# Kernel tuning notes

Measured on AMD Instinct MI355X. Metric: run time of the kernel, lower is better.

Reference implementation:

```python
import jax, jax.numpy as jnp
import numpy as np

B, S, D, H = 2, 2048, 2048, 16
HD = D // H  # 128
L = 10  # adapter_len


def setup_inputs() -> dict:
    key = jax.random.key(0)
    ks = jax.random.split(key, 8)
    x = jax.random.normal(ks[0], (B, S, D), dtype=jnp.float32)
    wq = jax.random.normal(ks[1], (D, D), dtype=jnp.float32) * 0.02
    wk = jax.random.normal(ks[2], (D, D), dtype=jnp.float32) * 0.02
    wv = jax.random.normal(ks[3], (D, D), dtype=jnp.float32) * 0.02
    wo = jax.random.normal(ks[4], (D, D), dtype=jnp.float32) * 0.02
    adapter = jax.random.normal(ks[5], (1, L, D), dtype=jnp.float32)
    gate = jax.random.normal(ks[6], (1, H, 1, 1), dtype=jnp.float32) * 0.1
    # rotary frequencies (LLaMA style, theta=10000)
    inv_freq = 1.0 / (10000.0 ** (jnp.arange(0, HD, 2, dtype=jnp.float32) / HD))
    t = jnp.arange(S, dtype=jnp.float32)
    ang = jnp.outer(t, inv_freq)  # [S, HD//2]
    freqs_cos = jnp.cos(ang)
    freqs_sin = jnp.sin(ang)
    # additive causal mask [1,1,S,S]
    mask = jnp.triu(jnp.full((S, S), -1e9, dtype=jnp.float32), k=1)[None, None]
    return {"x": x, "wq": wq, "wk": wk, "wv": wv, "wo": wo,
            "adapter": adapter, "gate": gate,
            "freqs_cos": freqs_cos, "freqs_sin": freqs_sin, "mask": mask}


def _rope(v, cos, sin):
    # v: [B,S,H,HD]; cos/sin: [S, HD//2]; complex multiply on (even, odd) pairs
    v = v.reshape(*v.shape[:-1], HD // 2, 2)
    v0, v1 = v[..., 0], v[..., 1]
    c = cos[None, :, None, :]
    s = sin[None, :, None, :]
    out = jnp.stack([v0 * c - v1 * s, v0 * s + v1 * c], axis=-1)
    return out.reshape(*out.shape[:-2], HD)


def reference(x, wq, wk, wv, wo, adapter, gate, freqs_cos, freqs_sin, mask):
    scale = 1.0 / np.sqrt(HD)
    xq = (x @ wq).reshape(B, S, H, HD)
    xk = (x @ wk).reshape(B, S, H, HD)
    xv = (x @ wv).reshape(B, S, H, HD)
    xq = _rope(xq, freqs_cos, freqs_sin)
    xk = _rope(xk, freqs_cos, freqs_sin)
    # self-attention with additive causal mask
    scores = jnp.einsum('bqhd,bkhd->bhqk', xq, xk) * scale + mask
    probs = jax.nn.softmax(scores.astype(jnp.float32), axis=-1).astype(xq.dtype)
    out = jnp.einsum('bhqk,bkhd->bqhd', probs, xv)  # [B,S,H,HD]
    # gated adapter cross-attention (no rotary on adapter K/V)
    ak = (adapter[0] @ wk).reshape(L, H, HD)
    av = (adapter[0] @ wv).reshape(L, H, HD)
    a_scores = jnp.einsum('bqhd,khd->bhqk', xq, ak) * scale
    a_probs = gate * jax.nn.softmax(a_scores.astype(jnp.float32), axis=-1).astype(xq.dtype)
    out = out + jnp.einsum('bhqk,khd->bqhd', a_probs, av)
    return out.reshape(B, S, D) @ wo
```

## Files before the change

### kernel.cpp

```cpp
#include <hip/hip_runtime.h>


typedef unsigned short ushort_t;
typedef unsigned int uint32;
typedef __attribute__((ext_vector_type(8))) short bf16x8;
typedef __attribute__((ext_vector_type(4))) float f32x4;

__device__ __forceinline__ void async16(void* lds, const void* g) {
  __builtin_amdgcn_global_load_lds((const __attribute__((address_space(1))) void*)g,
                                   (__attribute__((address_space(3))) void*)lds,
                                   16, 0, 0);
}
__device__ __forceinline__ ushort_t f2bf(float f) {
  uint32 u = __float_as_uint(f);
  u += 0x7FFFu + ((u >> 16) & 1u);
  return (ushort_t)(u >> 16);
}
__device__ __forceinline__ float bf2f(ushort_t b) {
  return __uint_as_float(((uint32)b) << 16);
}
__device__ __forceinline__ float dpp_xor1(float v) {
  return __int_as_float(__builtin_amdgcn_update_dpp(
      0, __float_as_int(v), 0xB1, 0xf, 0xf, true));
}
#define DPP_MAX(t, ctrl) \
  t = fmaxf(t, __int_as_float(__builtin_amdgcn_update_dpp( \
      0, __float_as_int(t), (ctrl), 0xf, 0xf, true)))
#define DPP_ADD(t, ctrl) \
  t += __int_as_float(__builtin_amdgcn_update_dpp( \
      0, __float_as_int(t), (ctrl), 0xf, 0xf, true))
__device__ __forceinline__ float rowmax16(float t) {
  DPP_MAX(t, 0xB1);
  DPP_MAX(t, 0x4E);
  t = fmaxf(t, __int_as_float(__builtin_amdgcn_ds_swizzle(
      __float_as_int(t), 0x101F)));
  DPP_MAX(t, 0x128);
  return t;
}
__device__ __forceinline__ float rowsum16(float t) {
  DPP_ADD(t, 0xB1);
  DPP_ADD(t, 0x4E);
  t += __int_as_float(__builtin_amdgcn_ds_swizzle(__float_as_int(t), 0x101F));
  DPP_ADD(t, 0x128);
  return t;
}

__global__ __launch_bounds__(256) void cast_x_kernel(const float* __restrict__ x,
                                                     ushort_t* __restrict__ Xb) {
  size_t i = ((size_t)blockIdx.x * 256 + threadIdx.x) * 8;
  float4 a = *(const float4*)(x + i);
  float4 b = *(const float4*)(x + i + 4);
  uint4 o;
  o.x = (uint32)f2bf(a.x) | ((uint32)f2bf(a.y) << 16);
  o.y = (uint32)f2bf(a.z) | ((uint32)f2bf(a.w) << 16);
  o.z = (uint32)f2bf(b.x) | ((uint32)f2bf(b.y) << 16);
  o.w = (uint32)f2bf(b.z) | ((uint32)f2bf(b.w) << 16);
  *(uint4*)(Xb + i) = o;
}

__global__ __launch_bounds__(256) void transpose_w_kernel(
    const float* __restrict__ w0, const float* __restrict__ w1,
    const float* __restrict__ w2, const float* __restrict__ w3,
    ushort_t* __restrict__ outBase) {
  const float* W = (blockIdx.z == 0) ? w0 : (blockIdx.z == 1) ? w1
                 : (blockIdx.z == 2) ? w2 : w3;
  ushort_t* Wt = outBase + (size_t)blockIdx.z * 4194304;
  __shared__ float L[64][65];
  int t = threadIdx.x, tc = t & 63, tr = t >> 6;
  int k0 = blockIdx.x * 64, n0 = blockIdx.y * 64;
  for (int i = 0; i < 16; ++i) {
    int r = i * 4 + tr;
    L[r][tc] = W[(size_t)(k0 + r) * 2048 + n0 + tc];
  }
  __syncthreads();
  int tr8 = t >> 5, tc2 = t & 31;
  for (int i = 0; i < 8; ++i) {
    int r = i * 8 + tr8;
    uint32 pk = (uint32)f2bf(L[2 * tc2][r]) | ((uint32)f2bf(L[2 * tc2 + 1][r]) << 16);
    *(uint32*)(Wt + (size_t)(n0 + r) * 2048 + k0 + 2 * tc2) = pk;
  }
}

__global__ __launch_bounds__(256) void adapter_kv_kernel(
    const float* __restrict__ adapter, const float* __restrict__ wk,
    const float* __restrict__ wv, float* __restrict__ ak, float* __restrict__ av) {
  const float* W = blockIdx.z ? wv : wk;
  float* out = blockIdx.z ? av : ak;
  __shared__ float As[10][128];
  int t = threadIdx.x;
  int k0 = blockIdx.y * 128;
  for (int i = t; i < 1280; i += 256)
    As[i >> 7][i & 127] = adapter[(size_t)(i >> 7) * 2048 + k0 + (i & 127)];
  __syncthreads();
  int n = blockIdx.x * 256 + t;
  float acc[10];
#pragma unroll
  for (int l = 0; l < 10; ++l) acc[l] = 0.f;
  for (int kk = 0; kk < 128; ++kk) {
    float wv_ = W[(size_t)(k0 + kk) * 2048 + n];
#pragma unroll
    for (int l = 0; l < 10; ++l) acc[l] += As[l][kk] * wv_;
  }
#pragma unroll
  for (int l = 0; l < 10; ++l) atomicAdd(&out[l * 2048 + n], acc[l]);
}

__global__ __launch_bounds__(256) void adapter_pack_kernel(
    const float* __restrict__ ak, const float* __restrict__ av,
    ushort_t* __restrict__ akb, ushort_t* __restrict__ avb) {
  int t = blockIdx.x * 256 + threadIdx.x;
  if (t < 32768) {
    int h = t >> 11, l = (t >> 7) & 15, d = t & 127;
    akb[t] = (l < 10) ? f2bf(ak[l * 2048 + h * 128 + d]) : (ushort_t)0;
  }
  int h = t >> 12, d = (t >> 5) & 127, l = t & 31;
  avb[t] = (l < 10) ? f2bf(av[l * 2048 + h * 128 + d]) : (ushort_t)0;
}

#define QK_BARX() asm volatile("s_barrier" ::: "memory")
#define QK_LGKM0() asm volatile("s_waitcnt lgkmcnt(0)" ::: "memory")

__global__ __launch_bounds__(512, 2) void gemm_qkv256_kernel(
    const ushort_t* __restrict__ A, const ushort_t* __restrict__ Bt,
    ushort_t* __restrict__ outQ, ushort_t* __restrict__ outK,
    ushort_t* __restrict__ Vt,
    const float* __restrict__ fc, const float* __restrict__ fs) {
  __shared__ char lds[131072];
  const int tid = (int)threadIdx.x;
  const int w = tid >> 6, lane = tid & 63, quad = lane >> 4, l15 = lane & 15;
  const int wr = w >> 2, wc = w & 3;
  const int nt = 32;

  const int wg = ((int)blockIdx.x & 7) * 48 + ((int)blockIdx.x >> 3);
  const size_t bm0 = (size_t)(wg & 15) * 256;
  const size_t bn0 = (size_t)(wg >> 4) * 256;

#define SEGH(OB, G, GROW, T, KH)                                               \
  do { if ((T) < nt) {                                                         \
    int c_ = lane & 3;                                                         \
    _Pragma("unroll") for (int L_ = 0; L_ < 2; ++L_) {                         \
      int r_ = L_ * 128 + w * 16 + (lane >> 2);                                \
      async16(lds + (OB) + (((T) & 1) * 32768) + (KH) * 16384 + L_ * 8192 + w * 1024, \
              (G) + ((GROW) + (size_t)r_) * 2048 +                             \
                  (size_t)((T) * 64 + (KH) * 32 + ((c_ ^ (r_ & 3)) * 8)));     \
    } } } while (0)
#define FRAG(OB, BUF, KS, RA) \
  (*(const bf16x8*)(lds + (OB) + (BUF) + (KS) * 16384 + (RA) * 64 + \
                    ((quad ^ ((RA) & 3)) * 16)))

  f32x4 acc[8][4];
  f32x4 z4 = {0.f, 0.f, 0.f, 0.f};
#pragma unroll
  for (int i = 0; i < 8; ++i)
#pragma unroll
    for (int j = 0; j < 4; ++j) acc[i][j] = z4;

  SEGH(0, A, bm0, 0, 0); SEGH(65536, Bt, bn0, 0, 0);
  SEGH(0, A, bm0, 0, 1); SEGH(65536, Bt, bn0, 0, 1);
  SEGH(0, A, bm0, 1, 0); SEGH(65536, Bt, bn0, 1, 0);
  asm volatile("s_waitcnt vmcnt(4)" ::: "memory");
  QK_BARX();

  for (int t = 0; t < nt; ++t) {
    const int buf = (t & 1) * 32768;
    bf16x8 af[4], bfv[4];

#pragma unroll
    for (int j = 0; j < 4; ++j) bfv[j] = FRAG(65536, buf, 0, wc * 64 + j * 16 + l15);
#pragma unroll
    for (int i = 0; i < 4; ++i) af[i] = FRAG(0, buf, 0, wr * 128 + i * 16 + l15);
    SEGH(0, A, bm0, t + 1, 1);
    QK_BARX();
    QK_LGKM0();
    __builtin_amdgcn_s_setprio(1);
#pragma unroll
    for (int i = 0; i < 4; ++i)
#pragma unroll
      for (int j = 0; j < 4; ++j)
        acc[i][j] = __builtin_amdgcn_mfma_f32_16x16x32_bf16(af[i], bfv[j], acc[i][j], 0, 0, 0);
    __builtin_amdgcn_s_setprio(0);
    QK_BARX();

#pragma unroll
    for (int i = 0; i < 4; ++i) af[i] = FRAG(0, buf, 0, wr * 128 + (4 + i) * 16 + l15);
    SEGH(65536, Bt, bn0, t + 1, 1);
    QK_BARX();
    QK_LGKM0();
    __builtin_amdgcn_s_setprio(1);
#pragma unroll
    for (int i = 0; i < 4; ++i)
#pragma unroll
      for (int j = 0; j < 4; ++j)
        acc[4 + i][j] = __builtin_amdgcn_mfma_f32_16x16x32_bf16(af[i], bfv[j], acc[4 + i][j], 0, 0, 0);
    __builtin_amdgcn_s_setprio(0);
    QK_BARX();

#pragma unroll
    for (int j = 0; j < 4; ++j) bfv[j] = FRAG(65536, buf, 1, wc * 64 + j * 16 + l15);
#pragma unroll
    for (int i = 0; i < 4; ++i) af[i] = FRAG(0, buf, 1, wr * 128 + (4 + i) * 16 + l15);
    SEGH(0, A, bm0, t + 2, 0);
    QK_BARX();
    QK_LGKM0();
    __builtin_amdgcn_s_setprio(1);
#pragma unroll
    for (int i = 0; i < 4; ++i)
#pragma unroll
      for (int j = 0; j < 4; ++j)
        acc[4 + i][j] = __builtin_amdgcn_mfma_f32_16x16x32_bf16(af[i], bfv[j], acc[4 + i][j], 0, 0, 0);
    __builtin_amdgcn_s_setprio(0);
    QK_BARX();

#pragma unroll
    for (int i = 0; i < 4; ++i) af[i] = FRAG(0, buf, 1, wr * 128 + i * 16 + l15);
    SEGH(65536, Bt, bn0, t + 2, 0);
    QK_BARX();
    QK_LGKM0();
    __builtin_amdgcn_s_setprio(1);
#pragma unroll
    for (int i = 0; i < 4; ++i)
#pragma unroll
      for (int j = 0; j < 4; ++j)
        acc[i][j] = __builtin_amdgcn_mfma_f32_16x16x32_bf16(af[i], bfv[j], acc[i][j], 0, 0, 0);
    __builtin_amdgcn_s_setprio(0);
    if (t == nt - 2) asm volatile("s_waitcnt vmcnt(0)" ::: "memory");
    else             asm volatile("s_waitcnt vmcnt(4)" ::: "memory");
    QK_BARX();
  }
#undef SEGH
#undef FRAG

  const int seg = (int)(bn0 >> 11);
  if (seg < 2) {
    ushort_t* ob = seg ? outK : outQ;
#pragma unroll
    for (int i = 0; i < 8; ++i)
#pragma unroll
      for (int r = 0; r < 4; ++r) {
        size_t m = bm0 + wr * 128 + i * 16 + quad * 4 + r;
        int s = (int)(m & 2047);
#pragma unroll
        for (int j = 0; j < 4; ++j) {
          size_t n = (bn0 + wc * 64 + j * 16 + l15) & 2047;
          float v = acc[i][j][r];
          float v2 = dpp_xor1(v);
          int fi = ((int)n & 127) >> 1;
          float cosv = fc[s * 64 + fi];
          float sinv = fs[s * 64 + fi];
          v = (lane & 1) ? (v2 * sinv + v * cosv) : (v * cosv - v2 * sinv);
          ob[m * 2048 + n] = f2bf(v);
        }
      }
  } else {
    char* T = lds + w * 16384;
    const int b = (int)(bm0 >> 11);
    const int n2 = (int)(bn0 & 2047) + wc * 64;
#pragma unroll
    for (int mh = 0; mh < 2; ++mh) {
#pragma unroll
      for (int i = 0; i < 4; ++i)
#pragma unroll
        for (int j = 0; j < 4; ++j) {
          int nn = j * 16 + l15;
          int md0 = i * 8 + quad * 2;
          const f32x4 av4 = acc[mh * 4 + i][j];
          uint32 p01 = (uint32)f2bf(av4[0]) | ((uint32)f2bf(av4[1]) << 16);
          uint32 p23 = (uint32)f2bf(av4[2]) | ((uint32)f2bf(av4[3]) << 16);
          *(uint32*)(T + nn * 128 + ((md0 ^ (nn & 31)) * 4)) = p01;
          *(uint32*)(T + nn * 128 + (((md0 + 1) ^ (nn & 31)) * 4)) = p23;
        }
      const int s0 = (int)(bm0 & 2047) + wr * 128 + mh * 64;
#pragma unroll
      for (int it = 0; it < 32; ++it) {
        int row = it * 2 + (lane >> 5);
        int pp = lane & 31;
        uint32 dv = *(const uint32*)(T + row * 128 + pp * 4);
        int md = pp ^ (row & 31);
        int nloc = n2 + row;
        size_t bh = (size_t)b * 16 + (nloc >> 7);
        *(uint32*)(Vt + (bh * 128 + (size_t)(nloc & 127)) * 2048 + s0 + 2 * md) = dv;
      }
    }
  }
}

__device__ __forceinline__ void kloop_128x256(
    char* lds, const ushort_t* __restrict__ A, const ushort_t* __restrict__ Bt,
    size_t bm0, size_t bn0, f32x4 (&acc)[4][4]) {
  const int tid = (int)threadIdx.x;
  const int w = tid >> 6, lane = tid & 63, quad = lane >> 4, l15 = lane & 15;
  const int wr = (w >> 2) * 64, wc = (w & 3) * 64;
  const int nt = 32;
  char* const pA0 = lds;
  char* const pA1 = lds + 16384;
  char* const pB0 = lds + 32768;
  char* const pB1 = lds + 65536;

#define PAT(T) (((T) & 1) ? pA1 : pA0)
#define PBT(T) (((T) & 1) ? pB1 : pB0)
#define SEGL(OP, LDSB, GROW, T)                                                \
  do {                                                                         \
    int rr_ = w * 8 + (lane >> 3);                                             \
    int cl_ = (lane & 7) ^ (rr_ & 7);                                          \
    async16((LDSB) + w * 1024,                                                 \
            (OP) + ((GROW) + (size_t)rr_) * 2048 + (size_t)((T) * 64 + cl_ * 8)); \
  } while (0)
#define ST_A(T)                                                                \
  do { if ((T) < nt) { SEGL(A, PAT(T), bm0, (T));                              \
                       SEGL(A, PAT(T) + 8192, bm0 + 64, (T)); } } while (0)
#define ST_B0(T)                                                               \
  do { if ((T) < nt) SEGL(Bt, PBT(T), bn0, (T)); } while (0)
#define ST_B123(T)                                                             \
  do { if ((T) < nt) { SEGL(Bt, PBT(T) + 8192,  bn0 + 64,  (T));               \
                       SEGL(Bt, PBT(T) + 16384, bn0 + 128, (T));               \
                       SEGL(Bt, PBT(T) + 24576, bn0 + 192, (T)); } } while (0)

  ST_A(0); ST_B0(0); ST_B123(0); ST_B123(1);
  asm volatile("s_waitcnt vmcnt(3)" ::: "memory");
  QK_BARX();

#pragma unroll 2
  for (int t = 0; t < nt; ++t) {
    const char* pA = PAT(t);
    const char* pB = PBT(t);
    bf16x8 bfv[4][2];
#pragma unroll
    for (int j = 0; j < 4; ++j) {
      int brow = wc + j * 16 + l15;
#pragma unroll
      for (int ks = 0; ks < 2; ++ks)
        bfv[j][ks] = *(const bf16x8*)(pB + brow * 128 +
                                      (((ks * 4 + quad) ^ (brow & 7)) * 16));
    }
#pragma unroll
    for (int ph = 0; ph < 2; ++ph) {
      bf16x8 af[2][2];
#pragma unroll
      for (int ii = 0; ii < 2; ++ii) {
        int arow = wr + (ph * 2 + ii) * 16 + l15;
#pragma unroll
        for (int ks = 0; ks < 2; ++ks)
          af[ii][ks] = *(const bf16x8*)(pA + arow * 128 +
                                        (((ks * 4 + quad) ^ (arow & 7)) * 16));
      }
      if (ph == 0) { ST_A(t + 1); ST_B0(t + 1); }
      else         { ST_B123(t + 2); }
      QK_BARX();
      QK_LGKM0();
      __builtin_amdgcn_s_setprio(1);
#pragma unroll
      for (int ks = 0; ks < 2; ++ks)
#pragma unroll
        for (int ii = 0; ii < 2; ++ii)
#pragma unroll
          for (int j = 0; j < 4; ++j)
            acc[ph * 2 + ii][j] = __builtin_amdgcn_mfma_f32_16x16x32_bf16(
                af[ii][ks], bfv[j][ks], acc[ph * 2 + ii][j], 0, 0, 0);
      __builtin_amdgcn_s_setprio(0);
      if (ph == 1) {
        if (t == nt - 2) asm volatile("s_waitcnt vmcnt(0)" ::: "memory");
        else             asm volatile("s_waitcnt vmcnt(3)" ::: "memory");
      }
      QK_BARX();
    }
  }
#undef PAT
#undef PBT
#undef SEGL
#undef ST_A
#undef ST_B0
#undef ST_B123
}

__global__ __launch_bounds__(512, 2) void gemm_wo_kernel(
    const ushort_t* __restrict__ A, const ushort_t* __restrict__ Bt,
    float* __restrict__ out) {
  __shared__ char lds[98304];
  const int tid = (int)threadIdx.x;
  const int w = tid >> 6, lane = tid & 63, quad = lane >> 4, l15 = lane & 15;
  const int wr = (w >> 2) * 64, wc = (w & 3) * 64;

  const int wg = ((int)blockIdx.x & 7) * 32 + ((int)blockIdx.x >> 3);
  const size_t bm0 = (size_t)(wg & 31) * 128;
  const size_t bn0 = (size_t)(wg >> 5) * 256;

  f32x4 acc[4][4];
  f32x4 z4 = {0.f, 0.f, 0.f, 0.f};
#pragma unroll
  for (int i = 0; i < 4; ++i)
#pragma unroll
    for (int j = 0; j < 4; ++j) acc[i][j] = z4;

  kloop_128x256(lds, A, Bt, bm0, bn0, acc);

#pragma unroll
  for (int i = 0; i < 4; ++i)
#pragma unroll
    for (int r = 0; r < 4; ++r) {
      size_t m = bm0 + wr + i * 16 + quad * 4 + r;
#pragma unroll
      for (int j = 0; j < 4; ++j) {
        size_t n = bn0 + wc + j * 16 + l15;
        out[m * 2048 + n] = acc[i][j][r];
      }
    }
}

__global__ __launch_bounds__(256, 4) void flash_kernel(
    const ushort_t* __restrict__ Qb, const ushort_t* __restrict__ Kb,
    const ushort_t* __restrict__ Vt, const ushort_t* __restrict__ akb,
    const ushort_t* __restrict__ avb, const float* __restrict__ gate,
    ushort_t* __restrict__ Ob) {
  __shared__ char ldsK[16384];
  __shared__ char ldsV[16384];
  __shared__ char ldsP[8192];
  const int tid = threadIdx.x;
  const int w = tid >> 6, lane = tid & 63, quad = lane >> 4, l15 = lane & 15;
  const int idx = blockIdx.x;
  const int pg = idx >> 8, c = idx & 255;
  const int u = c >> 3, vv = c & 7;
  const int uu = (pg & 2) ? ((u + 16) & 31) : u;
  const int qt2 = (pg & 1) ? (31 - uu) : uu;
  const int hb = (pg << 3) | vv;
  const int h = hb >> 1, b = hb & 1;
  const float scale = 0.08838834764831845f;

  bf16x8 ones;
#pragma unroll
  for (int j = 0; j < 8; ++j) ones[j] = (short)0x3F80;

  bf16x8 qf[4];
  {
    size_t qrow = (size_t)qt2 * 64 + w * 16 + l15;
    const ushort_t* base = Qb + ((size_t)b * 2048 + qrow) * 2048 + h * 128 + quad * 8;
#pragma unroll
    for (int ds = 0; ds < 4; ++ds) qf[ds] = *(const bf16x8*)(base + ds * 32);
  }

  f32x4 zero4 = {0.f, 0.f, 0.f, 0.f};
  f32x4 oacc[8];
  f32x4 osum = zero4;
  float mrow[4];
#pragma unroll
  for (int n8 = 0; n8 < 8; ++n8) oacc[n8] = zero4;
#pragma unroll
  for (int r = 0; r < 4; ++r) mrow[r] = -1e30f;

  for (int kt = 0; kt <= qt2; ++kt) {
#pragma unroll
    for (int ii = 0; ii < 4; ++ii) {
      int r0 = w * 16 + ii * 4;
      int row = r0 + (lane >> 4);
      int cl = (lane & 15) ^ (row & 15);
      async16(ldsK + r0 * 256,
              Kb + ((size_t)b * 2048 + kt * 64 + row) * 2048 + h * 128 + cl * 8);
    }
#pragma unroll
    for (int ii = 0; ii < 4; ++ii) {
      int d0 = w * 32 + ii * 8;
      int dr = d0 + (lane >> 3);
      int cl = (lane & 7) ^ (dr & 7);
      async16(ldsV + d0 * 128,
              Vt + ((size_t)(b * 16 + h) * 128 + dr) * 2048 + kt * 64 + cl * 8);
    }
    __syncthreads();

    f32x4 sacc[4];
#pragma unroll
    for (int nt = 0; nt < 4; ++nt) sacc[nt] = zero4;
#pragma unroll
    for (int ds = 0; ds < 4; ++ds) {
      bf16x8 kf[4];
      int ch = ds * 4 + quad;
#pragma unroll
      for (int nt = 0; nt < 4; ++nt) {
        int row = nt * 16 + l15;
        kf[nt] = *(const bf16x8*)(ldsK + row * 256 + ((ch ^ (row & 15)) * 16));
      }
#pragma unroll
      for (int nt = 0; nt < 4; ++nt)
        sacc[nt] = __builtin_amdgcn_mfma_f32_16x16x32_bf16(qf[ds], kf[nt], sacc[nt], 0, 0, 0);
    }

    const bool domask = (kt == qt2);
    float tmax[4] = {-1e30f, -1e30f, -1e30f, -1e30f};
    const int qbr = qt2 * 64 + w * 16 + quad * 4;
#pragma unroll
    for (int nt = 0; nt < 4; ++nt) {
      int kg = kt * 64 + nt * 16 + l15;
#pragma unroll
      for (int r = 0; r < 4; ++r) {
        float s = sacc[nt][r] * scale;
        if (domask && kg > qbr + r) s = -1e30f;
        sacc[nt][r] = s;
        tmax[r] = fmaxf(tmax[r], s);
      }
    }
    float need = 0.f;
#pragma unroll
    for (int r = 0; r < 4; ++r) {
      tmax[r] = rowmax16(tmax[r]);
      need = fmaxf(need, tmax[r] - mrow[r]);
    }
    if (__any(need > 8.0f)) {
      float alpha[4];
#pragma unroll
      for (int r = 0; r < 4; ++r) {
        float mnew = fmaxf(mrow[r], tmax[r]);
        alpha[r] = __expf(mrow[r] - mnew);
        osum[r] *= alpha[r];
        mrow[r] = mnew;
      }
#pragma unroll
      for (int n8 = 0; n8 < 8; ++n8)
#pragma unroll
        for (int r = 0; r < 4; ++r) oacc[n8][r] *= alpha[r];
    }
    uint32 pk[4][4];
#pragma unroll
    for (int nt = 0; nt < 4; ++nt)
#pragma unroll
      for (int r = 0; r < 4; ++r) {
        float pv = __expf(sacc[nt][r] - mrow[r]);
        float pn = dpp_xor1(pv);
        uint32 d_;
        asm volatile("v_cvt_pk_bf16_f32 %0, %1, %2" : "=v"(d_) : "v"(pv), "v"(pn));
        pk[nt][r] = d_;
      }
    if (!(lane & 1)) {
#pragma unroll
      for (int nt = 0; nt < 4; ++nt)
#pragma unroll
        for (int r = 0; r < 4; ++r) {
          int col = nt * 16 + l15;
          int prow = w * 16 + quad * 4 + r;
          *(uint32*)(ldsP + prow * 128 + (((col >> 3) ^ (prow & 7)) * 16) + (col & 7) * 2) = pk[nt][r];
        }
    }

#pragma unroll
    for (int ks = 0; ks < 2; ++ks) {
      int ch = ks * 4 + quad;
      int prow = w * 16 + l15;
      bf16x8 pf = *(const bf16x8*)(ldsP + prow * 128 + ((ch ^ (prow & 7)) * 16));
      osum = __builtin_amdgcn_mfma_f32_16x16x32_bf16(pf, ones, osum, 0, 0, 0);
#pragma unroll
      for (int n8 = 0; n8 < 8; ++n8) {
        int dr = n8 * 16 + l15;
        bf16x8 vf = *(const bf16x8*)(ldsV + dr * 128 + ((ch ^ (dr & 7)) * 16));
        oacc[n8] = __builtin_amdgcn_mfma_f32_16x16x32_bf16(pf, vf, oacc[n8], 0, 0, 0);
      }
    }
    __syncthreads();
  }

  const float g = gate[h];
  {
    int row = w * 16 + (lane >> 2);
    *(uint2*)(ldsP + row * 80 + 32 + (lane & 3) * 8) = make_uint2(0, 0);
  }
  f32x4 sa = zero4;
#pragma unroll
  for (int ds = 0; ds < 4; ++ds) {
    bf16x8 kfa = *(const bf16x8*)(akb + ((size_t)h * 16 + l15) * 128 + ds * 32 + quad * 8);
    sa = __builtin_amdgcn_mfma_f32_16x16x32_bf16(qf[ds], kfa, sa, 0, 0, 0);
  }
#pragma unroll
  for (int r = 0; r < 4; ++r) {
    float s = sa[r] * scale;
    if (l15 >= 10) s = -1e30f;
    float mx = rowmax16(s);
    float e = __expf(s - mx);
    float sum = rowsum16(e);
    float pv = g * e / sum;
    int row = w * 16 + quad * 4 + r;
    *(ushort_t*)(ldsP + row * 80 + l15 * 2) = f2bf(pv);
  }
  bf16x8 paf = *(const bf16x8*)(ldsP + (w * 16 + l15) * 80 + quad * 16);

  float rl[4];
#pragma unroll
  for (int r = 0; r < 4; ++r) rl[r] = 1.f / osum[r];
#pragma unroll
  for (int n8 = 0; n8 < 8; ++n8)
#pragma unroll
    for (int r = 0; r < 4; ++r) oacc[n8][r] *= rl[r];
#pragma unroll
  for (int n8 = 0; n8 < 8; ++n8) {
    bf16x8 avf = *(const bf16x8*)(avb + ((size_t)h * 128 + n8 * 16 + l15) * 32 + quad * 8);
    oacc[n8] = __builtin_amdgcn_mfma_f32_16x16x32_bf16(paf, avf, oacc[n8], 0, 0, 0);
  }
  size_t qb0 = (size_t)qt2 * 64 + w * 16 + quad * 4;
#pragma unroll
  for (int n8 = 0; n8 < 8; ++n8) {
    size_t col = (size_t)h * 128 + n8 * 16 + l15;
#pragma unroll
    for (int r = 0; r < 4; ++r)
      Ob[((size_t)b * 2048 + qb0 + r) * 2048 + col] = f2bf(oacc[n8][r]);
  }
}

extern "C" void kernel_launch(void* const* d_in, const int* in_sizes, int n_in,
                              void* d_out, int out_size, void* d_ws, size_t ws_size,
                              hipStream_t stream) {
  (void)in_sizes; (void)n_in; (void)out_size; (void)ws_size;
  const float* x       = (const float*)d_in[0];
  const float* wq      = (const float*)d_in[1];
  const float* wk      = (const float*)d_in[2];
  const float* wv      = (const float*)d_in[3];
  const float* wo      = (const float*)d_in[4];
  const float* adapter = (const float*)d_in[5];
  const float* gate    = (const float*)d_in[6];
  const float* fc      = (const float*)d_in[7];
  const float* fs      = (const float*)d_in[8];

  char* ws = (char*)d_ws;
  ushort_t* Xb   = (ushort_t*)(ws + 0);
  ushort_t* WtQ  = (ushort_t*)(ws + 16777216);
  ushort_t* WtO  = (ushort_t*)(ws + 41943040);
  ushort_t* Qb   = (ushort_t*)(ws + 50331648);
  ushort_t* Kb   = (ushort_t*)(ws + 67108864);
  ushort_t* Vt   = (ushort_t*)(ws + 83886080);
  float*    ak   = (float*)   (ws + 100663296);
  float*    av   = (float*)   (ws + 100745216);
  ushort_t* akb  = (ushort_t*)(ws + 100827136);
  ushort_t* avb  = (ushort_t*)(ws + 100892672);
  ushort_t* Ob   = Xb;

  cast_x_kernel<<<4096, 256, 0, stream>>>(x, Xb);
  transpose_w_kernel<<<dim3(32, 32, 4), 256, 0, stream>>>(wq, wk, wv, wo, WtQ);
  hipMemsetAsync(ak, 0, 163840, stream);
  adapter_kv_kernel<<<dim3(8, 16, 2), 256, 0, stream>>>(adapter, wk, wv, ak, av);
  adapter_pack_kernel<<<256, 256, 0, stream>>>(ak, av, akb, avb);
  gemm_qkv256_kernel<<<dim3(384), 512, 0, stream>>>(Xb, WtQ, Qb, Kb, Vt, fc, fs);
  flash_kernel<<<dim3(1024), 256, 0, stream>>>(Qb, Kb, Vt, akb, avb, gate, Ob);
  gemm_wo_kernel<<<dim3(256), 512, 0, stream>>>(Ob, WtO, (float*)d_out);
}
```

Before: 454.8 us.

## Restructure QKV GEMM LDS layout to full-row 128B slices with 8-way XOR swizzle

Replaces the split-K-half LDS layout (two 64B half-tiles per row with a 4-way swizzle) with a contiguous 128-byte row layout using an 8-way XOR swizzle. The async global-to-LDS prefetch schedule is reorganised too: each stage loads a whole 64-row slice, the lookahead drops from two half-tiles to one full tile, and vmcnt waits move to new points. The goal is fewer LDS bank conflicts and more coalesced global loads. The shorter prefetch distance may expose more memory latency, and the buffer-reuse timing needs care.

```diff
diff --git a/kernel.cpp b/kernel.cpp
--- a/kernel.cpp
+++ b/kernel.cpp
@@ -135,18 +135,17 @@
   const size_t bm0 = (size_t)(wg & 15) * 256;
   const size_t bn0 = (size_t)(wg >> 4) * 256;
 
-#define SEGH(OB, G, GROW, T, KH)                                               \
+#define STSL(OB, G, GROW, T, S)                                                \
   do { if ((T) < nt) {                                                         \
-    int c_ = lane & 3;                                                         \
-    _Pragma("unroll") for (int L_ = 0; L_ < 2; ++L_) {                         \
-      int r_ = L_ * 128 + w * 16 + (lane >> 2);                                \
-      async16(lds + (OB) + (((T) & 1) * 32768) + (KH) * 16384 + L_ * 8192 + w * 1024, \
-              (G) + ((GROW) + (size_t)r_) * 2048 +                             \
-                  (size_t)((T) * 64 + (KH) * 32 + ((c_ ^ (r_ & 3)) * 8)));     \
-    } } } while (0)
+    int r_ = (S) * 64 + w * 8 + (lane >> 3);                                   \
+    int cl_ = (lane & 7) ^ (r_ & 7);                                           \
+    async16(lds + (OB) + (((T) & 1) * 32768) + (S) * 8192 + w * 1024,          \
+            (G) + ((GROW) + (size_t)r_) * 2048 +                               \
+                (size_t)((T) * 64 + cl_ * 8));                                 \
+  } } while (0)
 #define FRAG(OB, BUF, KS, RA) \
-  (*(const bf16x8*)(lds + (OB) + (BUF) + (KS) * 16384 + (RA) * 64 + \
-                    ((quad ^ ((RA) & 3)) * 16)))
+  (*(const bf16x8*)(lds + (OB) + (BUF) + (RA) * 128 + \
+                    ((((KS) * 4 + quad) ^ ((RA) & 7)) * 16)))
 
   f32x4 acc[8][4];
   f32x4 z4 = {0.f, 0.f, 0.f, 0.f};
@@ -155,10 +154,11 @@
 #pragma unroll
     for (int j = 0; j < 4; ++j) acc[i][j] = z4;
 
-  SEGH(0, A, bm0, 0, 0); SEGH(65536, Bt, bn0, 0, 0);
-  SEGH(0, A, bm0, 0, 1); SEGH(65536, Bt, bn0, 0, 1);
-  SEGH(0, A, bm0, 1, 0); SEGH(65536, Bt, bn0, 1, 0);
-  asm volatile("s_waitcnt vmcnt(4)" ::: "memory");
+  STSL(65536, Bt, bn0, 0, 0); STSL(65536, Bt, bn0, 0, 1);
+  STSL(65536, Bt, bn0, 0, 2); STSL(65536, Bt, bn0, 0, 3);
+  STSL(0, A, bm0, 0, 0); STSL(0, A, bm0, 0, 2);
+  STSL(0, A, bm0, 0, 1); STSL(0, A, bm0, 0, 3);
+  asm volatile("s_waitcnt vmcnt(2)" ::: "memory");
   QK_BARX();
 
   for (int t = 0; t < nt; ++t) {
@@ -169,7 +169,7 @@
     for (int j = 0; j < 4; ++j) bfv[j] = FRAG(65536, buf, 0, wc * 64 + j * 16 + l15);
 #pragma unroll
     for (int i = 0; i < 4; ++i) af[i] = FRAG(0, buf, 0, wr * 128 + i * 16 + l15);
-    SEGH(0, A, bm0, t + 1, 1);
+    STSL(65536, Bt, bn0, t + 1, 0); STSL(65536, Bt, bn0, t + 1, 1);
     QK_BARX();
     QK_LGKM0();
     __builtin_amdgcn_s_setprio(1);
@@ -179,11 +179,13 @@
       for (int j = 0; j < 4; ++j)
         acc[i][j] = __builtin_amdgcn_mfma_f32_16x16x32_bf16(af[i], bfv[j], acc[i][j], 0, 0, 0);
     __builtin_amdgcn_s_setprio(0);
+    if (t == nt - 1) asm volatile("s_waitcnt vmcnt(0)" ::: "memory");
+    else             asm volatile("s_waitcnt vmcnt(2)" ::: "memory");
     QK_BARX();
 
 #pragma unroll
     for (int i = 0; i < 4; ++i) af[i] = FRAG(0, buf, 0, wr * 128 + (4 + i) * 16 + l15);
-    SEGH(65536, Bt, bn0, t + 1, 1);
+    STSL(65536, Bt, bn0, t + 1, 2); STSL(65536, Bt, bn0, t + 1, 3);
     QK_BARX();
     QK_LGKM0();
     __builtin_amdgcn_s_setprio(1);
@@ -199,7 +201,7 @@
     for (int j = 0; j < 4; ++j) bfv[j] = FRAG(65536, buf, 1, wc * 64 + j * 16 + l15);
 #pragma unroll
     for (int i = 0; i < 4; ++i) af[i] = FRAG(0, buf, 1, wr * 128 + (4 + i) * 16 + l15);
-    SEGH(0, A, bm0, t + 2, 0);
+    STSL(0, A, bm0, t + 1, 0); STSL(0, A, bm0, t + 1, 2);
     QK_BARX();
     QK_LGKM0();
     __builtin_amdgcn_s_setprio(1);
@@ -213,7 +215,7 @@
 
 #pragma unroll
     for (int i = 0; i < 4; ++i) af[i] = FRAG(0, buf, 1, wr * 128 + i * 16 + l15);
-    SEGH(65536, Bt, bn0, t + 2, 0);
+    STSL(0, A, bm0, t + 1, 1); STSL(0, A, bm0, t + 1, 3);
     QK_BARX();
     QK_LGKM0();
     __builtin_amdgcn_s_setprio(1);
@@ -223,11 +225,10 @@
       for (int j = 0; j < 4; ++j)
         acc[i][j] = __builtin_amdgcn_mfma_f32_16x16x32_bf16(af[i], bfv[j], acc[i][j], 0, 0, 0);
     __builtin_amdgcn_s_setprio(0);
-    if (t == nt - 2) asm volatile("s_waitcnt vmcnt(0)" ::: "memory");
-    else             asm volatile("s_waitcnt vmcnt(4)" ::: "memory");
-    QK_BARX();
-  }
-#undef SEGH
+    asm volatile("s_waitcnt vmcnt(2)" ::: "memory");
+    QK_BARX();
+  }
+#undef STSL
 #undef FRAG
 
   const int seg = (int)(bn0 >> 11);
```

Measured after the change: 441.0 us. 3.0% less time.
